# Kernel tuning notes

Hardware: AMD Instinct MI355X
Metric: run time of the kernel (lower is better)

Reference implementation:

```python
import jax, jax.numpy as jnp
import numpy as np

DIM = 4096
N_HEADS = 32
N_KV_HEADS = 8
HEAD_DIM = DIM // N_HEADS  # 128
N_REP = N_HEADS // N_KV_HEADS  # 4
MAX_BS = 16
MAX_SEQ = 4096
SEQLEN = 1
START_POS = 4095
ROPE_THETA = 500000.0


def setup_inputs() -> dict:
    key = jax.random.key(0)
    ks = jax.random.split(key, 8)
    w_scale = 0.02  # keep logits in a sane range
    x = jax.random.normal(ks[0], (MAX_BS, SEQLEN, DIM), dtype=jnp.float32)
    wq = jax.random.normal(ks[1], (DIM, N_HEADS * HEAD_DIM), dtype=jnp.float32) * w_scale
    wk = jax.random.normal(ks[2], (DIM, N_KV_HEADS * HEAD_DIM), dtype=jnp.float32) * w_scale
    wv = jax.random.normal(ks[3], (DIM, N_KV_HEADS * HEAD_DIM), dtype=jnp.float32) * w_scale
    wo = jax.random.normal(ks[4], (N_HEADS * HEAD_DIM, DIM), dtype=jnp.float32) * w_scale
    cache_k = jax.random.normal(ks[5], (MAX_BS, MAX_SEQ, N_KV_HEADS, HEAD_DIM), dtype=jnp.float32)
    cache_v = jax.random.normal(ks[6], (MAX_BS, MAX_SEQ, N_KV_HEADS, HEAD_DIM), dtype=jnp.float32)
    # true rotary frequencies for positions [START_POS, START_POS+SEQLEN)
    inv_freq = 1.0 / (ROPE_THETA ** (np.arange(0, HEAD_DIM, 2, dtype=np.float32) / HEAD_DIM))  # [hd/2]
    t = np.arange(START_POS, START_POS + SEQLEN, dtype=np.float32)[:, None]  # [s,1]
    angles = t * inv_freq[None, :]  # [s, hd/2]
    freqs_cos = jnp.asarray(np.cos(angles), dtype=jnp.float32)
    freqs_sin = jnp.asarray(np.sin(angles), dtype=jnp.float32)
    return {"x": x, "wq": wq, "wk": wk, "wv": wv, "wo": wo,
            "cache_k": cache_k, "cache_v": cache_v,
            "freqs_cos": freqs_cos, "freqs_sin": freqs_sin,
            "start_pos": START_POS}


def _rope(t, cos, sin):
    # t: [b, s, h, hd]; cos/sin: [s, hd/2] -> broadcast [1, s, 1, hd/2]
    b, s, h, hd = t.shape
    tp = t.reshape(b, s, h, hd // 2, 2)
    e, o = tp[..., 0], tp[..., 1]
    c = cos[None, :, None, :]
    sn = sin[None, :, None, :]
    re = e * c - o * sn
    im = e * sn + o * c
    return jnp.stack([re, im], axis=-1).reshape(b, s, h, hd)


def reference(x, wq, wk, wv, wo, cache_k, cache_v, freqs_cos, freqs_sin, start_pos):
    bsz, seqlen, _ = x.shape
    xq = (x @ wq).reshape(bsz, seqlen, N_HEADS, HEAD_DIM)
    xk = (x @ wk).reshape(bsz, seqlen, N_KV_HEADS, HEAD_DIM)
    xv = (x @ wv).reshape(bsz, seqlen, N_KV_HEADS, HEAD_DIM)
    xq = _rope(xq, freqs_cos, freqs_sin)
    xk = _rope(xk, freqs_cos, freqs_sin)
    # KV-cache append
    cache_k = jax.lax.dynamic_update_slice(cache_k, xk, (0, start_pos, 0, 0))
    cache_v = jax.lax.dynamic_update_slice(cache_v, xv, (0, start_pos, 0, 0))
    kv_len = start_pos + seqlen  # static Python int
    keys = cache_k[:, :kv_len]    # [b, t, g, hd]
    values = cache_v[:, :kv_len]  # [b, t, g, hd]
    # GQA via broadcasting (math-equivalent to repeat_kv)
    q = xq.reshape(bsz, seqlen, N_KV_HEADS, N_REP, HEAD_DIM)
    scale = 1.0 / jnp.sqrt(jnp.float32(HEAD_DIM))
    scores = jnp.einsum('bsgrh,btgh->bgrst', q, keys) * scale  # [b,g,r,s,t]
    probs = jax.nn.softmax(scores.astype(jnp.float32), axis=-1).astype(xq.dtype)
    out = jnp.einsum('bgrst,btgh->bsgrh', probs, values)  # [b,s,g,r,hd]
    out = out.reshape(bsz, seqlen, N_HEADS * HEAD_DIM)
    return out @ wo
```

## Files before the change

kernel.cpp:

```cpp
#include <hip/hip_runtime.h>
#include <math.h>

#define DIM    4096
#define NH     32
#define NKV    8
#define HD     128
#define BS     16
#define KVLEN  4096
#define LASTPOS 4095
#define QKV_COLS 6144
#define NKC    64

typedef float f32x4 __attribute__((ext_vector_type(4)));

__device__ __forceinline__ f32x4 ntload4(const float* p) {
  return __builtin_nontemporal_load((const f32x4*)p);
}

#define WS_QKV   0
#define WS_ATTN  98304
#define WS_PART  163840
#define WS_PART2 8814592
#define WS_PQ    9084928
#define WS_PW    15376384

__global__ __launch_bounds__(256) void qkv_projA(
    const float* __restrict__ x, const float* __restrict__ wq,
    const float* __restrict__ wk, const float* __restrict__ wv,
    float* __restrict__ pq) {
  __shared__ float xs[16 * 64];
  const int tid = threadIdx.x;
  const int col = (blockIdx.x * 256 + tid) * 2;
  const int kc = blockIdx.y;
  const int k0 = kc * 64;

  for (int i = tid; i < 1024; i += 256) {
    int b = i >> 6, k = i & 63;
    xs[i] = x[b * DIM + k0 + k];
  }
  __syncthreads();

  const float* w;
  int wstride, wcol;
  if (col < 4096)      { w = wq; wstride = 4096; wcol = col; }
  else if (col < 5120) { w = wk; wstride = 1024; wcol = col - 4096; }
  else                 { w = wv; wstride = 1024; wcol = col - 5120; }
  const float* wp = w + (size_t)k0 * wstride + wcol;

  float acc0[16], acc1[16];
#pragma unroll
  for (int b = 0; b < 16; ++b) { acc0[b] = 0.f; acc1[b] = 0.f; }

#pragma unroll 2
  for (int k = 0; k < 64; k += 4) {
    float2 w0 = *(const float2*)(wp + (size_t)(k + 0) * wstride);
    float2 w1 = *(const float2*)(wp + (size_t)(k + 1) * wstride);
    float2 w2 = *(const float2*)(wp + (size_t)(k + 2) * wstride);
    float2 w3 = *(const float2*)(wp + (size_t)(k + 3) * wstride);
#pragma unroll
    for (int b = 0; b < 16; ++b) {
      float4 xb = *(const float4*)(&xs[b * 64 + k]);
      acc0[b] += xb.x * w0.x + xb.y * w1.x + xb.z * w2.x + xb.w * w3.x;
      acc1[b] += xb.x * w0.y + xb.y * w1.y + xb.z * w2.y + xb.w * w3.y;
    }
  }
#pragma unroll
  for (int b = 0; b < 16; ++b) {
    *(float2*)(&pq[((size_t)kc * 16 + b) * QKV_COLS + col]) = make_float2(acc0[b], acc1[b]);
  }
}

__global__ __launch_bounds__(256) void qkv_projB(
    const float* __restrict__ pq, float* __restrict__ qkv,
    const float* __restrict__ fc, const float* __restrict__ fs) {
  int t = blockIdx.x * 256 + threadIdx.x;
  int b = t / 3072, pr = t % 3072;
  int col = 2 * pr;
  float e = 0.f, o = 0.f;
#pragma unroll 8
  for (int kc = 0; kc < NKC; ++kc) {
    float2 v = *(const float2*)(&pq[((size_t)kc * 16 + b) * QKV_COLS + col]);
    e += v.x; o += v.y;
  }
  float re = e, im = o;
  if (col < 5120) {
    int i = (col & 127) >> 1;
    float c = fc[i], s = fs[i];
    float scale = (col < 4096) ? 0.08838834764831845f : 1.0f;
    re = (e * c - o * s) * scale;
    im = (e * s + o * c) * scale;
  }
  *(float2*)(&qkv[b * QKV_COLS + col]) = make_float2(re, im);
}

__global__ __launch_bounds__(256, 4) void attn_partial(
    const float* __restrict__ cache_k, const float* __restrict__ cache_v,
    const float* __restrict__ qkv, float* __restrict__ part) {
  const int tid = threadIdx.x;
  const int w = tid >> 6, lane = tid & 63;
  const int p = lane >> 4, ql = lane & 15;
  const int chunk = blockIdx.x & 31;
  const int bg = blockIdx.x >> 5;
  const int b = bg >> 3, g = bg & 7;
  const int unit = chunk * 4 + w;
  const int t0w = chunk * 128 + w * 32;

  const float* qbase = qkv + b * QKV_COLS + g * 512;
  f32x4 qA[4], qB[4];
#pragma unroll
  for (int h = 0; h < 4; ++h) {
    qA[h] = *(const f32x4*)(qbase + h * 128 + ql * 8);
    qB[h] = *(const f32x4*)(qbase + h * 128 + ql * 8 + 4);
  }

  const float* kbase = cache_k + ((size_t)b * 4096 * 8 + g) * 128;
  const float* xk    = qkv + b * QKV_COLS + 4096 + g * 128;

  float sv8[8];
#pragma unroll
  for (int it = 0; it < 8; ++it) {
    int t = t0w + it * 4 + p;
    const float* krow = (t == LASTPOS) ? xk : (kbase + (size_t)t * 1024);
    f32x4 k0 = ntload4(krow + ql * 8);
    f32x4 k1 = ntload4(krow + ql * 8 + 4);
    float s[4];
#pragma unroll
    for (int h = 0; h < 4; ++h) {
      s[h] = k0[0]*qA[h][0] + k0[1]*qA[h][1] + k0[2]*qA[h][2] + k0[3]*qA[h][3]
           + k1[0]*qB[h][0] + k1[1]*qB[h][1] + k1[2]*qB[h][2] + k1[3]*qB[h][3];
    }
#pragma unroll
    for (int off = 1; off < 16; off <<= 1) {
#pragma unroll
      for (int h = 0; h < 4; ++h) s[h] += __shfl_xor(s[h], off);
    }
    int hsel = ql & 3;
    float v = s[0];
    if (hsel == 1) v = s[1];
    if (hsel == 2) v = s[2];
    if (hsel == 3) v = s[3];
    sv8[it] = v;
  }

  float m = -1e30f;
#pragma unroll
  for (int it = 0; it < 8; ++it) m = fmaxf(m, sv8[it]);
  m = fmaxf(m, __shfl_xor(m, 16));
  m = fmaxf(m, __shfl_xor(m, 32));
  float l = 0.f;
#pragma unroll
  for (int it = 0; it < 8; ++it) { sv8[it] = __expf(sv8[it] - m); l += sv8[it]; }
  l += __shfl_xor(l, 16);
  l += __shfl_xor(l, 32);
  if (lane < 4) {
    size_t pi = ((size_t)(bg * 128 + unit) * 4 + lane) * 132;
    part[pi + 128] = m;
    part[pi + 129] = l;
  }

  const float* vbase = cache_v + ((size_t)b * 4096 * 8 + g) * 128;
  const float* xv    = qkv + b * QKV_COLS + 5120 + g * 128;
  const int h2 = lane >> 5;
  const int dq = lane & 31;
  f32x4 acc[4];
#pragma unroll
  for (int h = 0; h < 4; ++h) acc[h] = (f32x4)(0.f);

#pragma unroll
  for (int jj = 0; jj < 16; ++jj) {
    int lr = 2 * jj + h2;
    int t = t0w + lr;
    const float* vrow = (t == LASTPOS) ? xv : (vbase + (size_t)t * 1024);
    f32x4 vv = ntload4(vrow + dq * 4);
    float sreg = sv8[jj >> 1];
    int srcb = (lr & 3) << 4;
    float p0 = __shfl(sreg, srcb + 0);
    float p1 = __shfl(sreg, srcb + 1);
    float p2 = __shfl(sreg, srcb + 2);
    float p3 = __shfl(sreg, srcb + 3);
    acc[0] += p0 * vv;
    acc[1] += p1 * vv;
    acc[2] += p2 * vv;
    acc[3] += p3 * vv;
  }
#pragma unroll
  for (int h = 0; h < 4; ++h) {
    acc[h][0] += __shfl_xor(acc[h][0], 32);
    acc[h][1] += __shfl_xor(acc[h][1], 32);
    acc[h][2] += __shfl_xor(acc[h][2], 32);
    acc[h][3] += __shfl_xor(acc[h][3], 32);
  }
  if (lane < 32) {
#pragma unroll
    for (int h = 0; h < 4; ++h) {
      size_t pi = ((size_t)(bg * 128 + unit) * 4 + h) * 132;
      *(f32x4*)(&part[pi + dq * 4]) = acc[h];
    }
  }
}

__global__ __launch_bounds__(512) void attn_combine1(
    const float* __restrict__ part, float* __restrict__ part2) {
  const int bgs = blockIdx.x;
  const int bg = bgs >> 2, s = bgs & 3;
  const int tid = threadIdx.x;
  __shared__ float ml[32][4][2];
  for (int i = tid; i < 256; i += 512) {
    int u = i >> 3, h = (i >> 1) & 3, q = i & 1;
    ml[u][h][q] = part[((size_t)(bg * 128 + s * 32 + u) * 4 + h) * 132 + 128 + q];
  }
  __syncthreads();
  const int h = tid >> 7, d = tid & 127;
  float M = -1e30f;
#pragma unroll
  for (int u = 0; u < 32; ++u) M = fmaxf(M, ml[u][h][0]);
  float num = 0.f, den = 0.f;
#pragma unroll 4
  for (int u = 0; u < 32; ++u) {
    float wgt = __expf(ml[u][h][0] - M);
    num += wgt * part[((size_t)(bg * 128 + s * 32 + u) * 4 + h) * 132 + d];
    den += wgt * ml[u][h][1];
  }
  size_t po = ((size_t)bgs * 4 + h) * 132;
  part2[po + d] = num;
  if (d == 0) { part2[po + 128] = M; part2[po + 129] = den; }
}

__global__ __launch_bounds__(256) void attn_combine2(
    const float* __restrict__ part2, float* __restrict__ attn_out) {
  int t = blockIdx.x * 256 + threadIdx.x;
  int d = t & 127, h = (t >> 7) & 3, bg = t >> 9;
  int b = bg >> 3, g = bg & 7;
  float ms[4];
  float M = -1e30f;
#pragma unroll
  for (int s = 0; s < 4; ++s) {
    ms[s] = part2[((size_t)(bg * 4 + s) * 4 + h) * 132 + 128];
    M = fmaxf(M, ms[s]);
  }
  float num = 0.f, den = 0.f;
#pragma unroll
  for (int s = 0; s < 4; ++s) {
    const float* pr = part2 + ((size_t)(bg * 4 + s) * 4 + h) * 132;
    float wgt = __expf(ms[s] - M);
    num += wgt * pr[d];
    den += wgt * pr[129];
  }
  attn_out[b * DIM + (g * 4 + h) * 128 + d] = num / den;
}

__global__ __launch_bounds__(256) void out_projA(
    const float* __restrict__ attn, const float* __restrict__ wo,
    float* __restrict__ pw) {
  __shared__ float xs[16 * 64];
  const int tid = threadIdx.x;
  const int col = (blockIdx.x * 256 + tid) * 2;
  const int kc = blockIdx.y;
  const int k0 = kc * 64;

  for (int i = tid; i < 1024; i += 256) {
    int b = i >> 6, k = i & 63;
    xs[i] = attn[b * DIM + k0 + k];
  }
  __syncthreads();

  const float* wp = wo + (size_t)k0 * 4096 + col;
  float acc0[16], acc1[16];
#pragma unroll
  for (int b = 0; b < 16; ++b) { acc0[b] = 0.f; acc1[b] = 0.f; }

#pragma unroll 2
  for (int k = 0; k < 64; k += 4) {
    float2 w0 = *(const float2*)(wp + (size_t)(k + 0) * 4096);
    float2 w1 = *(const float2*)(wp + (size_t)(k + 1) * 4096);
    float2 w2 = *(const float2*)(wp + (size_t)(k + 2) * 4096);
    float2 w3 = *(const float2*)(wp + (size_t)(k + 3) * 4096);
#pragma unroll
    for (int b = 0; b < 16; ++b) {
      float4 xb = *(const float4*)(&xs[b * 64 + k]);
      acc0[b] += xb.x * w0.x + xb.y * w1.x + xb.z * w2.x + xb.w * w3.x;
      acc1[b] += xb.x * w0.y + xb.y * w1.y + xb.z * w2.y + xb.w * w3.y;
    }
  }
#pragma unroll
  for (int b = 0; b < 16; ++b) {
    *(float2*)(&pw[((size_t)kc * 16 + b) * DIM + col]) = make_float2(acc0[b], acc1[b]);
  }
}

__global__ __launch_bounds__(256) void out_projB(
    const float* __restrict__ pw, float* __restrict__ out) {
  int t = blockIdx.x * 256 + threadIdx.x;
  int b = t >> 12, col = t & 4095;
  float sum = 0.f;
#pragma unroll 8
  for (int kc = 0; kc < NKC; ++kc)
    sum += pw[((size_t)kc * 16 + b) * DIM + col];
  out[b * DIM + col] = sum;
}

extern "C" void kernel_launch(void* const* d_in, const int* in_sizes, int n_in,
                              void* d_out, int out_size, void* d_ws, size_t ws_size,
                              hipStream_t stream) {
  const float* x  = (const float*)d_in[0];
  const float* wq = (const float*)d_in[1];
  const float* wk = (const float*)d_in[2];
  const float* wv = (const float*)d_in[3];
  const float* wo = (const float*)d_in[4];
  const float* ck = (const float*)d_in[5];
  const float* cv = (const float*)d_in[6];
  const float* fc = (const float*)d_in[7];
  const float* fs = (const float*)d_in[8];

  float* ws_f  = (float*)d_ws;
  float* qkv   = ws_f + WS_QKV;
  float* attn  = ws_f + WS_ATTN;
  float* part  = ws_f + WS_PART;
  float* part2 = ws_f + WS_PART2;
  float* pq    = ws_f + WS_PQ;
  float* pw    = ws_f + WS_PW;
  float* out   = (float*)d_out;

  qkv_projA<<<dim3(12, NKC), 256, 0, stream>>>(x, wq, wk, wv, pq);
  qkv_projB<<<192, 256, 0, stream>>>(pq, qkv, fc, fs);
  attn_partial<<<4096, 256, 0, stream>>>(ck, cv, qkv, part);
  attn_combine1<<<512, 512, 0, stream>>>(part, part2);
  attn_combine2<<<256, 256, 0, stream>>>(part2, attn);
  out_projA<<<dim3(8, NKC), 256, 0, stream>>>(attn, wo, pw);
  out_projB<<<256, 256, 0, stream>>>(pw, out);
}
```

Measured before the change: 194.6 us.

## Fuse per-block split-softmax reduction into attention kernel and drop combine pass

Each attention block now merges its four wave partials through shared memory before writing one partial per block, so the first combine kernel goes away and only a single 32-way combine kernel remains. This cuts partial-buffer traffic and removes a kernel launch, at the cost of a block-wide barrier inside the attention kernel. K and q loads are also changed to a split-half layout for coalescing, and the nontemporal load hints are swapped for plain loads, which may change cache behaviour on the streamed KV cache.

Measured after the change: 195.2 us. About the same (+0.3%).

```diff
diff --git a/kernel.cpp b/kernel.cpp
--- a/kernel.cpp
+++ b/kernel.cpp
@@ -13,16 +13,11 @@
 
 typedef float f32x4 __attribute__((ext_vector_type(4)));
 
-__device__ __forceinline__ f32x4 ntload4(const float* p) {
-  return __builtin_nontemporal_load((const f32x4*)p);
-}
-
 #define WS_QKV   0
 #define WS_ATTN  98304
 #define WS_PART  163840
-#define WS_PART2 8814592
-#define WS_PQ    9084928
-#define WS_PW    15376384
+#define WS_PQ    2326528
+#define WS_PW    8617984
 
 __global__ __launch_bounds__(256) void qkv_projA(
     const float* __restrict__ x, const float* __restrict__ wq,
@@ -96,21 +91,21 @@
 __global__ __launch_bounds__(256, 4) void attn_partial(
     const float* __restrict__ cache_k, const float* __restrict__ cache_v,
     const float* __restrict__ qkv, float* __restrict__ part) {
+  __shared__ float red[4][4][130];
   const int tid = threadIdx.x;
   const int w = tid >> 6, lane = tid & 63;
   const int p = lane >> 4, ql = lane & 15;
   const int chunk = blockIdx.x & 31;
   const int bg = blockIdx.x >> 5;
   const int b = bg >> 3, g = bg & 7;
-  const int unit = chunk * 4 + w;
   const int t0w = chunk * 128 + w * 32;
 
   const float* qbase = qkv + b * QKV_COLS + g * 512;
   f32x4 qA[4], qB[4];
 #pragma unroll
   for (int h = 0; h < 4; ++h) {
-    qA[h] = *(const f32x4*)(qbase + h * 128 + ql * 8);
-    qB[h] = *(const f32x4*)(qbase + h * 128 + ql * 8 + 4);
+    qA[h] = *(const f32x4*)(qbase + h * 128 + ql * 4);
+    qB[h] = *(const f32x4*)(qbase + h * 128 + 64 + ql * 4);
   }
 
   const float* kbase = cache_k + ((size_t)b * 4096 * 8 + g) * 128;
@@ -121,8 +116,8 @@
   for (int it = 0; it < 8; ++it) {
     int t = t0w + it * 4 + p;
     const float* krow = (t == LASTPOS) ? xk : (kbase + (size_t)t * 1024);
-    f32x4 k0 = ntload4(krow + ql * 8);
-    f32x4 k1 = ntload4(krow + ql * 8 + 4);
+    f32x4 k0 = *(const f32x4*)(krow + ql * 4);
+    f32x4 k1 = *(const f32x4*)(krow + 64 + ql * 4);
     float s[4];
 #pragma unroll
     for (int h = 0; h < 4; ++h) {
@@ -152,11 +147,6 @@
   for (int it = 0; it < 8; ++it) { sv8[it] = __expf(sv8[it] - m); l += sv8[it]; }
   l += __shfl_xor(l, 16);
   l += __shfl_xor(l, 32);
-  if (lane < 4) {
-    size_t pi = ((size_t)(bg * 128 + unit) * 4 + lane) * 132;
-    part[pi + 128] = m;
-    part[pi + 129] = l;
-  }
 
   const float* vbase = cache_v + ((size_t)b * 4096 * 8 + g) * 128;
   const float* xv    = qkv + b * QKV_COLS + 5120 + g * 128;
@@ -171,7 +161,7 @@
     int lr = 2 * jj + h2;
     int t = t0w + lr;
     const float* vrow = (t == LASTPOS) ? xv : (vbase + (size_t)t * 1024);
-    f32x4 vv = ntload4(vrow + dq * 4);
+    f32x4 vv = *(const f32x4*)(vrow + dq * 4);
     float sreg = sv8[jj >> 1];
     int srcb = (lr & 3) << 4;
     float p0 = __shfl(sreg, srcb + 0);
@@ -192,57 +182,47 @@
   }
   if (lane < 32) {
 #pragma unroll
-    for (int h = 0; h < 4; ++h) {
-      size_t pi = ((size_t)(bg * 128 + unit) * 4 + h) * 132;
-      *(f32x4*)(&part[pi + dq * 4]) = acc[h];
-    }
-  }
-}
-
-__global__ __launch_bounds__(512) void attn_combine1(
-    const float* __restrict__ part, float* __restrict__ part2) {
-  const int bgs = blockIdx.x;
-  const int bg = bgs >> 2, s = bgs & 3;
-  const int tid = threadIdx.x;
-  __shared__ float ml[32][4][2];
-  for (int i = tid; i < 256; i += 512) {
-    int u = i >> 3, h = (i >> 1) & 3, q = i & 1;
-    ml[u][h][q] = part[((size_t)(bg * 128 + s * 32 + u) * 4 + h) * 132 + 128 + q];
-  }
+    for (int h = 0; h < 4; ++h)
+      *(f32x4*)(&red[w][h][dq * 4]) = acc[h];
+  }
+  if (lane < 4) { red[w][lane][128] = m; red[w][lane][129] = l; }
   __syncthreads();
-  const int h = tid >> 7, d = tid & 127;
-  float M = -1e30f;
-#pragma unroll
-  for (int u = 0; u < 32; ++u) M = fmaxf(M, ml[u][h][0]);
-  float num = 0.f, den = 0.f;
-#pragma unroll 4
-  for (int u = 0; u < 32; ++u) {
-    float wgt = __expf(ml[u][h][0] - M);
-    num += wgt * part[((size_t)(bg * 128 + s * 32 + u) * 4 + h) * 132 + d];
-    den += wgt * ml[u][h][1];
-  }
-  size_t po = ((size_t)bgs * 4 + h) * 132;
-  part2[po + d] = num;
-  if (d == 0) { part2[po + 128] = M; part2[po + 129] = den; }
-}
-
-__global__ __launch_bounds__(256) void attn_combine2(
-    const float* __restrict__ part2, float* __restrict__ attn_out) {
+
+  for (int item = tid; item < 512; item += 256) {
+    int h = item >> 7, d = item & 127;
+    float M = -1e30f;
+#pragma unroll
+    for (int w2 = 0; w2 < 4; ++w2) M = fmaxf(M, red[w2][h][128]);
+    float num = 0.f, den = 0.f;
+#pragma unroll
+    for (int w2 = 0; w2 < 4; ++w2) {
+      float wgt = __expf(red[w2][h][128] - M);
+      num += wgt * red[w2][h][d];
+      den += wgt * red[w2][h][129];
+    }
+    size_t pi = ((size_t)blockIdx.x * 4 + h) * 132;
+    part[pi + d] = num;
+    if (d == 0) { part[pi + 128] = M; part[pi + 129] = den; }
+  }
+}
+
+__global__ __launch_bounds__(256) void attn_combine(
+    const float* __restrict__ part, float* __restrict__ attn_out) {
   int t = blockIdx.x * 256 + threadIdx.x;
   int d = t & 127, h = (t >> 7) & 3, bg = t >> 9;
   int b = bg >> 3, g = bg & 7;
-  float ms[4];
   float M = -1e30f;
-#pragma unroll
-  for (int s = 0; s < 4; ++s) {
-    ms[s] = part2[((size_t)(bg * 4 + s) * 4 + h) * 132 + 128];
-    M = fmaxf(M, ms[s]);
+  float ms[32];
+#pragma unroll
+  for (int c = 0; c < 32; ++c) {
+    ms[c] = part[((size_t)(bg * 32 + c) * 4 + h) * 132 + 128];
+    M = fmaxf(M, ms[c]);
   }
   float num = 0.f, den = 0.f;
-#pragma unroll
-  for (int s = 0; s < 4; ++s) {
-    const float* pr = part2 + ((size_t)(bg * 4 + s) * 4 + h) * 132;
-    float wgt = __expf(ms[s] - M);
+#pragma unroll 4
+  for (int c = 0; c < 32; ++c) {
+    const float* pr = part + ((size_t)(bg * 32 + c) * 4 + h) * 132;
+    float wgt = __expf(ms[c] - M);
     num += wgt * pr[d];
     den += wgt * pr[129];
   }
@@ -316,7 +296,6 @@
   float* qkv   = ws_f + WS_QKV;
   float* attn  = ws_f + WS_ATTN;
   float* part  = ws_f + WS_PART;
-  float* part2 = ws_f + WS_PART2;
   float* pq    = ws_f + WS_PQ;
   float* pw    = ws_f + WS_PW;
   float* out   = (float*)d_out;
@@ -324,8 +303,7 @@
   qkv_projA<<<dim3(12, NKC), 256, 0, stream>>>(x, wq, wk, wv, pq);
   qkv_projB<<<192, 256, 0, stream>>>(pq, qkv, fc, fs);
   attn_partial<<<4096, 256, 0, stream>>>(ck, cv, qkv, part);
-  attn_combine1<<<512, 512, 0, stream>>>(part, part2);
-  attn_combine2<<<256, 256, 0, stream>>>(part2, attn);
+  attn_combine<<<256, 256, 0, stream>>>(part, attn);
   out_projA<<<dim3(8, NKC), 256, 0, stream>>>(attn, wo, pw);
   out_projB<<<256, 256, 0, stream>>>(pw, out);
 }
```
